# Optimization experiments

Hardware: AMD Instinct MI355X
Metric: run time of the kernel (lower is better)

The kernel has to match this reference:

```python
import jax, jax.numpy as jnp
import numpy as np

NUM_LAYER = 5
EMB = 256
N = 100000
E = 300000
SELF_LOOP_BOND = 4
BN_EPS = 1e-5


def setup_inputs() -> dict:
    key = jax.random.key(0)
    ks = jax.random.split(key, 16)
    f = lambda k, shape: jax.random.normal(k, shape, jnp.float32) * 0.02
    return {
        "x_atom": jax.random.randint(ks[0], (N,), 0, 120),
        "x_chir": jax.random.randint(ks[1], (N,), 0, 3),
        "edge_index": jax.random.randint(ks[2], (2, E), 0, N),
        "edge_bond": jax.random.randint(ks[3], (E,), 0, 4),
        "edge_dir": jax.random.randint(ks[4], (E,), 0, 3),
        "atom_emb": f(ks[5], (120, EMB)),
        "chir_emb": f(ks[6], (3, EMB)),
        "bond_embs": f(ks[7], (NUM_LAYER, 6, EMB)),
        "dir_embs": f(ks[8], (NUM_LAYER, 3, EMB)),
        "W1s": f(ks[9], (NUM_LAYER, 2 * EMB, EMB)),
        "b1s": f(ks[10], (NUM_LAYER, 2 * EMB)),
        "W2s": f(ks[11], (NUM_LAYER, EMB, 2 * EMB)),
        "b2s": f(ks[12], (NUM_LAYER, EMB)),
        "bn_w": jnp.ones((NUM_LAYER, EMB), jnp.float32),
        "bn_b": jnp.zeros((NUM_LAYER, EMB), jnp.float32),
    }


def reference(x_atom, x_chir, edge_index, edge_bond, edge_dir,
              atom_emb, chir_emb, bond_embs, dir_embs,
              W1s, b1s, W2s, b2s, bn_w, bn_b):
    n = x_atom.shape[0]
    src, dst = edge_index[0], edge_index[1]
    # add self loops (edge_attr = [4, 0] for each node)
    loop = jnp.arange(n)
    src_full = jnp.concatenate([src, loop])          # [E+N]
    dst_full = jnp.concatenate([dst, loop])          # [E+N]
    bond_full = jnp.concatenate([edge_bond, jnp.full((n,), SELF_LOOP_BOND, edge_bond.dtype)])
    dir_full = jnp.concatenate([edge_dir, jnp.zeros((n,), edge_dir.dtype)])

    # initial node features: atom + chirality embeddings
    h = atom_emb[x_atom] + chir_emb[x_chir]          # [N, EMB]

    for l in range(NUM_LAYER):
        # per-layer edge embeddings (bond type + bond direction)
        e_emb = bond_embs[l][bond_full] + dir_embs[l][dir_full]   # [E+N, EMB]
        # message = x_j + edge_attr; aggregate = scatter-add to dst
        msg = h[src_full] + e_emb                                  # gather
        agg = jax.ops.segment_sum(msg, dst_full, num_segments=n)  # scatter-add
        # update MLP: Linear(EMB->2EMB) -> ReLU -> Linear(2EMB->EMB)
        hmid = jax.nn.relu(agg @ W1s[l].T + b1s[l])                # [N, 2EMB]
        h2 = hmid @ W2s[l].T + b2s[l]                              # [N, EMB]
        # batch norm (training mode: batch statistics, biased variance)
        mean = h2.mean(axis=0)
        var = h2.var(axis=0)
        h2 = (h2 - mean) * jax.lax.rsqrt(var + BN_EPS) * bn_w[l] + bn_b[l]
        # relu on all but last layer; dropout with p=0 is identity
        if l < NUM_LAYER - 1:
            h2 = jax.nn.relu(h2)
        h = h2
    # JK == 'last'
    return h
```

## Files before the change

kernel.cpp:

```cpp
#include <hip/hip_runtime.h>

#define EMB 256
#define NLAYER 5
#define CHUNK 1024

typedef unsigned int u32;
typedef unsigned short u16;

typedef __bf16 bf16x8 __attribute__((ext_vector_type(8)));
typedef float f32x4 __attribute__((ext_vector_type(4)));

__device__ __forceinline__ float bf2f(u16 u) {
    union { u32 i; float f; } x; x.i = ((u32)u) << 16; return x.f;
}
__device__ __forceinline__ u16 f2bf(float f) {
    union { float f; u32 i; } x; x.f = f;
    u32 r = x.i + 0x7FFFu + ((x.i >> 16) & 1u);
    return (u16)(r >> 16);
}
__device__ __forceinline__ void unpack4(uint2 p, float* o) {
    union { u32 i; float f; } a, b, c, d;
    a.i = p.x << 16; b.i = p.x & 0xFFFF0000u;
    c.i = p.y << 16; d.i = p.y & 0xFFFF0000u;
    o[0] = a.f; o[1] = b.f; o[2] = c.f; o[3] = d.f;
}

__global__ void k_detect(const u32* __restrict__ bnw_raw, int* __restrict__ flag) {
    if (threadIdx.x == 0 && blockIdx.x == 0)
        *flag = (bnw_raw[0] == 0x3F803F80u) ? 1 : 0;
}

struct Cvt { const void* s; u16* d; int n; };
struct CvtTab { Cvt t[10]; };

__global__ void k_convert(CvtTab tab, const int* __restrict__ flag, int maxn) {
    int f = *flag;
    int stride = gridDim.x * blockDim.x;
    for (int i = blockIdx.x * blockDim.x + threadIdx.x; i < maxn; i += stride) {
        for (int j = 0; j < 10; j++) {
            if (i < tab.t[j].n) {
                u16 v;
                if (f) v = ((const u16*)tab.t[j].s)[i];
                else   v = f2bf(((const float*)tab.t[j].s)[i]);
                tab.t[j].d[i] = v;
            }
        }
    }
}

__global__ void k_zero(u32* p, int n) {
    int i = blockIdx.x * blockDim.x + threadIdx.x;
    if (i < n) p[i] = 0u;
}

__global__ void k_hist(const int* __restrict__ eidx, const int* __restrict__ ebond,
                       const int* __restrict__ edir,
                       u32* __restrict__ cnt, u32* __restrict__ cntb, u32* __restrict__ cntd, int E) {
    int e = blockIdx.x * blockDim.x + threadIdx.x;
    if (e >= E) return;
    int dst = eidx[E + e];
    atomicAdd(&cnt[dst], 1u);
    atomicAdd(&cntb[dst * 4 + ebond[e]], 1u);
    atomicAdd(&cntd[dst * 3 + edir[e]], 1u);
}

__global__ void k_chunksum(const u32* __restrict__ cnt, u32* __restrict__ partial, int N) {
    int b = blockIdx.x, t = threadIdx.x;
    int base = b * CHUNK + t * 4;
    u32 s = 0;
    for (int i = 0; i < 4; i++) { int idx = base + i; if (idx < N) s += cnt[idx]; }
    __shared__ u32 red[256];
    red[t] = s; __syncthreads();
    for (int o = 128; o > 0; o >>= 1) { if (t < o) red[t] += red[t + o]; __syncthreads(); }
    if (t == 0) partial[b] = red[0];
}

__global__ void k_scanpartial(u32* partial, u32* indptr, int nch, int N) {
    if (threadIdx.x == 0 && blockIdx.x == 0) {
        u32 run = 0;
        for (int i = 0; i < nch; i++) { u32 x = partial[i]; partial[i] = run; run += x; }
        indptr[N] = run;
    }
}

__global__ void k_chunkscan(const u32* __restrict__ cnt, const u32* __restrict__ partial,
                            u32* __restrict__ indptr, u32* __restrict__ fillp, int N) {
    int b = blockIdx.x, t = threadIdx.x;
    int base = b * CHUNK + t * 4;
    u32 c[4]; u32 tsum = 0;
    for (int i = 0; i < 4; i++) { int idx = base + i; c[i] = (idx < N) ? cnt[idx] : 0u; tsum += c[i]; }
    __shared__ u32 sc[256];
    sc[t] = tsum; __syncthreads();
    for (int o = 1; o < 256; o <<= 1) {
        u32 x = (t >= o) ? sc[t - o] : 0u;
        __syncthreads();
        sc[t] += x;
        __syncthreads();
    }
    u32 run = partial[b] + sc[t] - tsum;
    for (int i = 0; i < 4; i++) {
        int idx = base + i;
        if (idx < N) { indptr[idx] = run; fillp[idx] = run; }
        run += c[i];
    }
}

__global__ void k_fill(const int* __restrict__ eidx, u32* __restrict__ fillp,
                       u32* __restrict__ srcs, int E) {
    int e = blockIdx.x * blockDim.x + threadIdx.x;
    if (e >= E) return;
    int dst = eidx[E + e];
    u32 pos = atomicAdd(&fillp[dst], 1u);
    srcs[pos] = (u32)eidx[e];
}

__global__ void k_h0(const int* __restrict__ xa, const int* __restrict__ xc,
                     const u16* __restrict__ aemb, const u16* __restrict__ cemb,
                     u16* __restrict__ H, int N) {
    int wave = threadIdx.x >> 6, lane = threadIdx.x & 63;
    int v = blockIdx.x * 4 + wave;
    if (v >= N) return;
    int a = xa[v], c = xc[v];
    int c4 = lane * 4;
    uint2 pa = *(const uint2*)(aemb + (size_t)a * EMB + c4);
    uint2 pc = *(const uint2*)(cemb + (size_t)c * EMB + c4);
    float fa[4], fc[4];
    unpack4(pa, fa); unpack4(pc, fc);
    ushort4 ov;
    ov.x = f2bf(fa[0] + fc[0]); ov.y = f2bf(fa[1] + fc[1]);
    ov.z = f2bf(fa[2] + fc[2]); ov.w = f2bf(fa[3] + fc[3]);
    *(ushort4*)(H + (size_t)v * EMB + c4) = ov;
}

__global__ void k_scatter(const u16* __restrict__ H, const u32* __restrict__ indptr,
                          const u32* __restrict__ srcs,
                          const u32* __restrict__ cntb, const u32* __restrict__ cntd,
                          const u16* __restrict__ bemb, const u16* __restrict__ demb,
                          const float* __restrict__ scsh, int relu,
                          u16* __restrict__ AGG, int N) {
    int wave = threadIdx.x >> 6, lane = threadIdx.x & 63;
    int v = blockIdx.x * 4 + wave;
    if (v >= N) return;
    int c4 = lane * 4;
    float sc[4] = {1.f, 1.f, 1.f, 1.f}, sh[4] = {0.f, 0.f, 0.f, 0.f};
    if (scsh) {
        float4 s0 = *(const float4*)(scsh + c4);
        float4 s1 = *(const float4*)(scsh + 256 + c4);
        sc[0] = s0.x; sc[1] = s0.y; sc[2] = s0.z; sc[3] = s0.w;
        sh[0] = s1.x; sh[1] = s1.y; sh[2] = s1.z; sh[3] = s1.w;
    }
    float acc[4] = {0.f, 0.f, 0.f, 0.f};
    u32 beg = indptr[v], end = indptr[v + 1];
    for (u32 e = beg; e < end; e++) {
        u32 s = srcs[e];
        uint2 p = *(const uint2*)(H + (size_t)s * EMB + c4);
        float f[4]; unpack4(p, f);
        for (int i = 0; i < 4; i++) {
            float y = f[i] * sc[i] + sh[i];
            if (relu) y = fmaxf(y, 0.f);
            acc[i] += y;
        }
    }
    {
        uint2 p = *(const uint2*)(H + (size_t)v * EMB + c4);
        float f[4]; unpack4(p, f);
        for (int i = 0; i < 4; i++) {
            float y = f[i] * sc[i] + sh[i];
            if (relu) y = fmaxf(y, 0.f);
            acc[i] += y;
        }
    }
    float cb[5];
    cb[0] = (float)cntb[v * 4 + 0]; cb[1] = (float)cntb[v * 4 + 1];
    cb[2] = (float)cntb[v * 4 + 2]; cb[3] = (float)cntb[v * 4 + 3]; cb[4] = 1.f;
    float cd[3];
    cd[0] = (float)cntd[v * 3 + 0] + 1.f; cd[1] = (float)cntd[v * 3 + 1]; cd[2] = (float)cntd[v * 3 + 2];
    for (int b = 0; b < 5; b++) {
        uint2 p = *(const uint2*)(bemb + b * EMB + c4);
        float f[4]; unpack4(p, f);
        for (int i = 0; i < 4; i++) acc[i] += cb[b] * f[i];
    }
    for (int d = 0; d < 3; d++) {
        uint2 p = *(const uint2*)(demb + d * EMB + c4);
        float f[4]; unpack4(p, f);
        for (int i = 0; i < 4; i++) acc[i] += cd[d] * f[i];
    }
    ushort4 ov;
    ov.x = f2bf(acc[0]); ov.y = f2bf(acc[1]); ov.z = f2bf(acc[2]); ov.w = f2bf(acc[3]);
    *(ushort4*)(AGG + (size_t)v * EMB + c4) = ov;
}

#define KP1 264
#define KB1 40

__global__ __launch_bounds__(256) void k_gemm1(
    const u16* __restrict__ A, const u16* __restrict__ W1, const u16* __restrict__ bias,
    u16* __restrict__ HM, int M) {
    __shared__ __align__(16) u16 As[128 * KP1];
    __shared__ __align__(16) u16 Bs[128 * KB1];
    int m0 = blockIdx.x * 128;
    int t = threadIdx.x;
    int wave = t >> 6, lane = t & 63;
    int wm = (wave >> 1) * 64, wn = (wave & 1) * 64;
    int lr = lane & 15, quad = lane >> 4;

    for (int it = 0; it < 16; it++) {
        int ci = t + it * 256;
        int r = ci >> 5, kc = (ci & 31) * 8;
        int gr = m0 + r; if (gr > M - 1) gr = M - 1;
        *(uint4*)(As + r * KP1 + kc) = *(const uint4*)(A + (size_t)gr * 256 + kc);
    }
    __syncthreads();

    for (int nc = 0; nc < 4; nc++) {
        int n0 = nc * 128;
        f32x4 acc[4][4];
        for (int i = 0; i < 4; i++)
            for (int j = 0; j < 4; j++)
                acc[i][j] = (f32x4){0.f, 0.f, 0.f, 0.f};
        for (int ks = 0; ks < 256; ks += 32) {
            __syncthreads();
            for (int it = 0; it < 2; it++) {
                int ci = t + it * 256;
                int r = ci >> 2, kc = (ci & 3) * 8;
                *(uint4*)(Bs + r * KB1 + kc) = *(const uint4*)(W1 + (size_t)(n0 + r) * 256 + ks + kc);
            }
            __syncthreads();
            bf16x8 af[4], bfr[4];
            for (int i = 0; i < 4; i++)
                af[i] = *(const bf16x8*)(As + (wm + i * 16 + lr) * KP1 + ks + quad * 8);
            for (int j = 0; j < 4; j++)
                bfr[j] = *(const bf16x8*)(Bs + (wn + j * 16 + lr) * KB1 + quad * 8);
            for (int i = 0; i < 4; i++)
                for (int j = 0; j < 4; j++)
                    acc[i][j] = __builtin_amdgcn_mfma_f32_16x16x32_bf16(af[i], bfr[j], acc[i][j], 0, 0, 0);
        }
        for (int j = 0; j < 4; j++) {
            int gn = n0 + wn + j * 16 + lr;
            float bv = bf2f(bias[gn]);
            for (int i = 0; i < 4; i++) {
                int mbase = m0 + wm + i * 16 + quad * 4;
                for (int r = 0; r < 4; r++) {
                    int gm = mbase + r;
                    if (gm < M) {
                        float v = fmaxf(acc[i][j][r] + bv, 0.f);
                        HM[(size_t)gm * 512 + gn] = f2bf(v);
                    }
                }
            }
        }
    }
}

#define LSTR 80

__global__ __launch_bounds__(256) void k_gemm2(
    const u16* __restrict__ A, const u16* __restrict__ B, const u16* __restrict__ bias,
    u16* __restrict__ C, float* __restrict__ S, int M) {
    __shared__ __align__(16) u16 As[128 * LSTR];
    __shared__ __align__(16) u16 Bs[128 * LSTR];
    int n0 = blockIdx.x * 128;
    int m0 = blockIdx.y * 128;
    int t = threadIdx.x;
    int wave = t >> 6, lane = t & 63;
    int wm = (wave >> 1) * 64, wn = (wave & 1) * 64;
    int lr = lane & 15, quad = lane >> 4;

    f32x4 acc[4][4];
    for (int i = 0; i < 4; i++)
        for (int j = 0; j < 4; j++)
            acc[i][j] = (f32x4){0.f, 0.f, 0.f, 0.f};

    for (int k0 = 0; k0 < 512; k0 += 64) {
        for (int it = 0; it < 4; it++) {
            int ci = t + it * 256;
            int r = ci >> 3, kc = (ci & 7) * 8;
            int gr = m0 + r; if (gr > M - 1) gr = M - 1;
            *(uint4*)(As + r * LSTR + kc) = *(const uint4*)(A + (size_t)gr * 512 + k0 + kc);
            *(uint4*)(Bs + r * LSTR + kc) = *(const uint4*)(B + (size_t)(n0 + r) * 512 + k0 + kc);
        }
        __syncthreads();
        for (int ks = 0; ks < 64; ks += 32) {
            bf16x8 af[4], bfr[4];
            for (int i = 0; i < 4; i++)
                af[i] = *(const bf16x8*)(As + (wm + i * 16 + lr) * LSTR + ks + quad * 8);
            for (int j = 0; j < 4; j++)
                bfr[j] = *(const bf16x8*)(Bs + (wn + j * 16 + lr) * LSTR + ks + quad * 8);
            for (int i = 0; i < 4; i++)
                for (int j = 0; j < 4; j++)
                    acc[i][j] = __builtin_amdgcn_mfma_f32_16x16x32_bf16(af[i], bfr[j], acc[i][j], 0, 0, 0);
        }
        __syncthreads();
    }
    for (int j = 0; j < 4; j++) {
        int gn = n0 + wn + j * 16 + lr;
        float bv = bf2f(bias[gn]);
        float s = 0.f, q = 0.f;
        for (int i = 0; i < 4; i++) {
            int mbase = m0 + wm + i * 16 + quad * 4;
            for (int r = 0; r < 4; r++) {
                int gm = mbase + r;
                if (gm < M) {
                    float v = acc[i][j][r] + bv;
                    C[(size_t)gm * 256 + gn] = f2bf(v);
                    s += v; q += v * v;
                }
            }
        }
        s += __shfl_xor(s, 16, 64); s += __shfl_xor(s, 32, 64);
        q += __shfl_xor(q, 16, 64); q += __shfl_xor(q, 32, 64);
        if (quad == 0) {
            atomicAdd(&S[gn], s);
            atomicAdd(&S[256 + gn], q);
        }
    }
}

__global__ void k_finalize(const float* __restrict__ S, const u16* __restrict__ bnw,
                           const u16* __restrict__ bnb, float* __restrict__ scsh, float invN) {
    int c = threadIdx.x;
    float mean = S[c] * invN;
    float var = S[256 + c] * invN - mean * mean;
    var = fmaxf(var, 0.f);
    float inv = rsqrtf(var + 1e-5f);
    float sc = bf2f(bnw[c]) * inv;
    scsh[c] = sc;
    scsh[256 + c] = bf2f(bnb[c]) - mean * sc;
}

__global__ void k_out(const u16* __restrict__ H2, const float* __restrict__ scsh,
                      void* __restrict__ out, const int* __restrict__ flag, int N) {
    int wave = threadIdx.x >> 6, lane = threadIdx.x & 63;
    int v = blockIdx.x * 4 + wave;
    if (v >= N) return;
    int c4 = lane * 4;
    float4 s0 = *(const float4*)(scsh + c4);
    float4 s1 = *(const float4*)(scsh + 256 + c4);
    uint2 p = *(const uint2*)(H2 + (size_t)v * EMB + c4);
    float f[4]; unpack4(p, f);
    float o0 = f[0] * s0.x + s1.x;
    float o1 = f[1] * s0.y + s1.y;
    float o2 = f[2] * s0.z + s1.z;
    float o3 = f[3] * s0.w + s1.w;
    if (*flag) {
        ushort4 ov;
        ov.x = f2bf(o0); ov.y = f2bf(o1); ov.z = f2bf(o2); ov.w = f2bf(o3);
        *(ushort4*)((u16*)out + (size_t)v * EMB + c4) = ov;
    } else {
        float4 ov = make_float4(o0, o1, o2, o3);
        *(float4*)((float*)out + (size_t)v * EMB + c4) = ov;
    }
}

extern "C" void kernel_launch(void* const* d_in, const int* in_sizes, int n_in,
                              void* d_out, int out_size, void* d_ws, size_t ws_size,
                              hipStream_t stream) {
    const int* x_atom = (const int*)d_in[0];
    const int* x_chir = (const int*)d_in[1];
    const int* eidx   = (const int*)d_in[2];
    const int* ebond  = (const int*)d_in[3];
    const int* edir   = (const int*)d_in[4];

    const int N = in_sizes[0];
    const int E = in_sizes[3];

    char* p = (char*)d_ws;
    size_t off = 0;
    auto alloc = [&](size_t bytes) -> void* {
        void* r = p + off;
        off += bytes;
        off = (off + 255) & ~(size_t)255;
        return r;
    };
    u16* X   = (u16*)alloc((size_t)N * EMB * 2);
    u16* Y   = (u16*)alloc((size_t)N * EMB * 2);
    u16* HM  = (u16*)alloc((size_t)N * 512 * 2);
    u32* cz  = (u32*)alloc(((size_t)8 * N + NLAYER * 512) * 4);
    u32* cnt  = cz;
    u32* cntb = cz + N;
    u32* cntd = cz + 5 * (size_t)N;
    float* stats5 = (float*)(cz + 8 * (size_t)N);
    u32* indptr = (u32*)alloc((size_t)(N + 1) * 4);
    u32* fillp  = (u32*)alloc((size_t)N * 4);
    u32* srcs   = (u32*)alloc((size_t)E * 4);
    u32* partial = (u32*)alloc(256 * 4);
    float* scsh  = (float*)alloc(512 * 4);
    int* flag    = (int*)alloc(256);

    int csz[10] = {120 * EMB, 3 * EMB, NLAYER * 6 * EMB, NLAYER * 3 * EMB,
                   NLAYER * 512 * EMB, NLAYER * 512, NLAYER * EMB * 512, NLAYER * EMB,
                   NLAYER * EMB, NLAYER * EMB};
    u16* cbuf[10];
    for (int j = 0; j < 10; j++) cbuf[j] = (u16*)alloc((size_t)csz[j] * 2);
    u16* atom_emb  = cbuf[0];
    u16* chir_emb  = cbuf[1];
    u16* bond_embs = cbuf[2];
    u16* dir_embs  = cbuf[3];
    u16* W1s = cbuf[4];
    u16* b1s = cbuf[5];
    u16* W2s = cbuf[6];
    u16* b2s = cbuf[7];
    u16* bnw = cbuf[8];
    u16* bnb = cbuf[9];

    const int nodeBlocks = (N + 3) / 4;
    const int nch = (N + CHUNK - 1) / CHUNK;

    k_detect<<<1, 64, 0, stream>>>((const u32*)d_in[13], flag);
    {
        CvtTab tab;
        int maxn = 0;
        for (int j = 0; j < 10; j++) {
            tab.t[j].s = d_in[5 + j];
            tab.t[j].d = cbuf[j];
            tab.t[j].n = csz[j];
            if (csz[j] > maxn) maxn = csz[j];
        }
        k_convert<<<(maxn + 255) / 256, 256, 0, stream>>>(tab, flag, maxn);
    }

    {
        int z = 8 * N + NLAYER * 512;
        k_zero<<<(z + 255) / 256, 256, 0, stream>>>(cz, z);
    }
    k_hist<<<(E + 255) / 256, 256, 0, stream>>>(eidx, ebond, edir, cnt, cntb, cntd, E);
    k_chunksum<<<nch, 256, 0, stream>>>(cnt, partial, N);
    k_scanpartial<<<1, 64, 0, stream>>>(partial, indptr, nch, N);
    k_chunkscan<<<nch, 256, 0, stream>>>(cnt, partial, indptr, fillp, N);
    k_fill<<<(E + 255) / 256, 256, 0, stream>>>(eidx, fillp, srcs, E);

    k_h0<<<nodeBlocks, 256, 0, stream>>>(x_atom, x_chir, atom_emb, chir_emb, X, N);

    u16* H = X;
    u16* A = Y;
    const int mTiles = (N + 127) / 128;
    for (int l = 0; l < NLAYER; l++) {
        const u16* bemb = bond_embs + (size_t)l * 6 * EMB;
        const u16* demb = dir_embs + (size_t)l * 3 * EMB;
        const u16* W1 = W1s + (size_t)l * 512 * EMB;
        const u16* B1 = b1s + (size_t)l * 512;
        const u16* W2 = W2s + (size_t)l * EMB * 512;
        const u16* B2 = b2s + (size_t)l * EMB;
        float* stats = stats5 + (size_t)l * 512;

        k_scatter<<<nodeBlocks, 256, 0, stream>>>(H, indptr, srcs, cntb, cntd, bemb, demb,
                                                  (l == 0) ? nullptr : scsh, (l == 0) ? 0 : 1,
                                                  A, N);
        k_gemm1<<<mTiles, 256, 0, stream>>>(A, W1, B1, HM, N);
        {
            dim3 g(2, mTiles);
            k_gemm2<<<g, 256, 0, stream>>>(HM, W2, B2, A, stats, N);
        }
        k_finalize<<<1, 256, 0, stream>>>(stats, bnw + (size_t)l * EMB, bnb + (size_t)l * EMB,
                                          scsh, 1.0f / (float)N);
        u16* tmp = H; H = A; A = tmp;
    }

    k_out<<<nodeBlocks, 256, 0, stream>>>(H, scsh, d_out, flag, N);
}
```

Baseline: 1.284 ms.

## Restructure GEMM tiling to 64-row blocks with direct global B loads and slotted BN stats

```diff
diff --git a/kernel.cpp b/kernel.cpp
--- a/kernel.cpp
+++ b/kernel.cpp
@@ -3,6 +3,7 @@
 #define EMB 256
 #define NLAYER 5
 #define CHUNK 1024
+#define NSLOT 64
 
 typedef unsigned int u32;
 typedef unsigned short u16;
@@ -191,20 +192,17 @@
 }
 
 #define KP1 264
-#define KB1 40
-
-__global__ __launch_bounds__(256) void k_gemm1(
+
+__global__ __launch_bounds__(256, 2) void k_gemm1(
     const u16* __restrict__ A, const u16* __restrict__ W1, const u16* __restrict__ bias,
     u16* __restrict__ HM, int M) {
-    __shared__ __align__(16) u16 As[128 * KP1];
-    __shared__ __align__(16) u16 Bs[128 * KB1];
-    int m0 = blockIdx.x * 128;
+    __shared__ __align__(16) u16 As[64 * KP1];
+    int m0 = blockIdx.x * 64;
     int t = threadIdx.x;
     int wave = t >> 6, lane = t & 63;
-    int wm = (wave >> 1) * 64, wn = (wave & 1) * 64;
     int lr = lane & 15, quad = lane >> 4;
 
-    for (int it = 0; it < 16; it++) {
+    for (int it = 0; it < 8; it++) {
         int ci = t + it * 256;
         int r = ci >> 5, kc = (ci & 31) * 8;
         int gr = m0 + r; if (gr > M - 1) gr = M - 1;
@@ -212,92 +210,78 @@
     }
     __syncthreads();
 
-    for (int nc = 0; nc < 4; nc++) {
-        int n0 = nc * 128;
-        f32x4 acc[4][4];
+    int nbase = wave * 128;
+    f32x4 acc[4][8];
+    for (int i = 0; i < 4; i++)
+        for (int j = 0; j < 8; j++)
+            acc[i][j] = (f32x4){0.f, 0.f, 0.f, 0.f};
+
+    for (int ks = 0; ks < 256; ks += 32) {
+        bf16x8 af[4], bfr[8];
         for (int i = 0; i < 4; i++)
-            for (int j = 0; j < 4; j++)
-                acc[i][j] = (f32x4){0.f, 0.f, 0.f, 0.f};
-        for (int ks = 0; ks < 256; ks += 32) {
-            __syncthreads();
-            for (int it = 0; it < 2; it++) {
-                int ci = t + it * 256;
-                int r = ci >> 2, kc = (ci & 3) * 8;
-                *(uint4*)(Bs + r * KB1 + kc) = *(const uint4*)(W1 + (size_t)(n0 + r) * 256 + ks + kc);
+            af[i] = *(const bf16x8*)(As + (i * 16 + lr) * KP1 + ks + quad * 8);
+        for (int j = 0; j < 8; j++)
+            bfr[j] = *(const bf16x8*)(W1 + (size_t)(nbase + j * 16 + lr) * 256 + ks + quad * 8);
+        for (int i = 0; i < 4; i++)
+            for (int j = 0; j < 8; j++)
+                acc[i][j] = __builtin_amdgcn_mfma_f32_16x16x32_bf16(af[i], bfr[j], acc[i][j], 0, 0, 0);
+    }
+    for (int j = 0; j < 8; j++) {
+        int gn = nbase + j * 16 + lr;
+        float bv = bf2f(bias[gn]);
+        for (int i = 0; i < 4; i++) {
+            int mbase = m0 + i * 16 + quad * 4;
+            for (int r = 0; r < 4; r++) {
+                int gm = mbase + r;
+                if (gm < M)
+                    HM[(size_t)gm * 512 + gn] = f2bf(fmaxf(acc[i][j][r] + bv, 0.f));
             }
-            __syncthreads();
-            bf16x8 af[4], bfr[4];
-            for (int i = 0; i < 4; i++)
-                af[i] = *(const bf16x8*)(As + (wm + i * 16 + lr) * KP1 + ks + quad * 8);
-            for (int j = 0; j < 4; j++)
-                bfr[j] = *(const bf16x8*)(Bs + (wn + j * 16 + lr) * KB1 + quad * 8);
-            for (int i = 0; i < 4; i++)
-                for (int j = 0; j < 4; j++)
-                    acc[i][j] = __builtin_amdgcn_mfma_f32_16x16x32_bf16(af[i], bfr[j], acc[i][j], 0, 0, 0);
-        }
-        for (int j = 0; j < 4; j++) {
-            int gn = n0 + wn + j * 16 + lr;
-            float bv = bf2f(bias[gn]);
-            for (int i = 0; i < 4; i++) {
-                int mbase = m0 + wm + i * 16 + quad * 4;
-                for (int r = 0; r < 4; r++) {
-                    int gm = mbase + r;
-                    if (gm < M) {
-                        float v = fmaxf(acc[i][j][r] + bv, 0.f);
-                        HM[(size_t)gm * 512 + gn] = f2bf(v);
-                    }
-                }
-            }
-        }
-    }
-}
-
-#define LSTR 80
-
-__global__ __launch_bounds__(256) void k_gemm2(
-    const u16* __restrict__ A, const u16* __restrict__ B, const u16* __restrict__ bias,
+        }
+    }
+}
+
+#define KP2 520
+
+__global__ __launch_bounds__(256, 2) void k_gemm2(
+    const u16* __restrict__ A, const u16* __restrict__ W2, const u16* __restrict__ bias,
     u16* __restrict__ C, float* __restrict__ S, int M) {
-    __shared__ __align__(16) u16 As[128 * LSTR];
-    __shared__ __align__(16) u16 Bs[128 * LSTR];
-    int n0 = blockIdx.x * 128;
-    int m0 = blockIdx.y * 128;
+    __shared__ __align__(16) u16 As[64 * KP2];
+    int m0 = blockIdx.x * 64;
     int t = threadIdx.x;
     int wave = t >> 6, lane = t & 63;
-    int wm = (wave >> 1) * 64, wn = (wave & 1) * 64;
     int lr = lane & 15, quad = lane >> 4;
 
+    for (int it = 0; it < 16; it++) {
+        int ci = t + it * 256;
+        int r = ci >> 6, kc = (ci & 63) * 8;
+        int gr = m0 + r; if (gr > M - 1) gr = M - 1;
+        *(uint4*)(As + r * KP2 + kc) = *(const uint4*)(A + (size_t)gr * 512 + kc);
+    }
+    __syncthreads();
+
+    int nbase = wave * 64;
     f32x4 acc[4][4];
     for (int i = 0; i < 4; i++)
         for (int j = 0; j < 4; j++)
             acc[i][j] = (f32x4){0.f, 0.f, 0.f, 0.f};
 
-    for (int k0 = 0; k0 < 512; k0 += 64) {
-        for (int it = 0; it < 4; it++) {
-            int ci = t + it * 256;
-            int r = ci >> 3, kc = (ci & 7) * 8;
-            int gr = m0 + r; if (gr > M - 1) gr = M - 1;
-            *(uint4*)(As + r * LSTR + kc) = *(const uint4*)(A + (size_t)gr * 512 + k0 + kc);
-            *(uint4*)(Bs + r * LSTR + kc) = *(const uint4*)(B + (size_t)(n0 + r) * 512 + k0 + kc);
-        }
-        __syncthreads();
-        for (int ks = 0; ks < 64; ks += 32) {
-            bf16x8 af[4], bfr[4];
-            for (int i = 0; i < 4; i++)
-                af[i] = *(const bf16x8*)(As + (wm + i * 16 + lr) * LSTR + ks + quad * 8);
+    for (int ks = 0; ks < 512; ks += 32) {
+        bf16x8 af[4], bfr[4];
+        for (int i = 0; i < 4; i++)
+            af[i] = *(const bf16x8*)(As + (i * 16 + lr) * KP2 + ks + quad * 8);
+        for (int j = 0; j < 4; j++)
+            bfr[j] = *(const bf16x8*)(W2 + (size_t)(nbase + j * 16 + lr) * 512 + ks + quad * 8);
+        for (int i = 0; i < 4; i++)
             for (int j = 0; j < 4; j++)
-                bfr[j] = *(const bf16x8*)(Bs + (wn + j * 16 + lr) * LSTR + ks + quad * 8);
-            for (int i = 0; i < 4; i++)
-                for (int j = 0; j < 4; j++)
-                    acc[i][j] = __builtin_amdgcn_mfma_f32_16x16x32_bf16(af[i], bfr[j], acc[i][j], 0, 0, 0);
-        }
-        __syncthreads();
-    }
+                acc[i][j] = __builtin_amdgcn_mfma_f32_16x16x32_bf16(af[i], bfr[j], acc[i][j], 0, 0, 0);
+    }
+    float* Sslot = S + (size_t)(blockIdx.x & (NSLOT - 1)) * 512;
     for (int j = 0; j < 4; j++) {
-        int gn = n0 + wn + j * 16 + lr;
+        int gn = nbase + j * 16 + lr;
         float bv = bf2f(bias[gn]);
         float s = 0.f, q = 0.f;
         for (int i = 0; i < 4; i++) {
-            int mbase = m0 + wm + i * 16 + quad * 4;
+            int mbase = m0 + i * 16 + quad * 4;
             for (int r = 0; r < 4; r++) {
                 int gm = mbase + r;
                 if (gm < M) {
@@ -310,8 +294,8 @@
         s += __shfl_xor(s, 16, 64); s += __shfl_xor(s, 32, 64);
         q += __shfl_xor(q, 16, 64); q += __shfl_xor(q, 32, 64);
         if (quad == 0) {
-            atomicAdd(&S[gn], s);
-            atomicAdd(&S[256 + gn], q);
+            atomicAdd(&Sslot[gn], s);
+            atomicAdd(&Sslot[256 + gn], q);
         }
     }
 }
@@ -319,8 +303,13 @@
 __global__ void k_finalize(const float* __restrict__ S, const u16* __restrict__ bnw,
                            const u16* __restrict__ bnb, float* __restrict__ scsh, float invN) {
     int c = threadIdx.x;
-    float mean = S[c] * invN;
-    float var = S[256 + c] * invN - mean * mean;
+    float sum = 0.f, sq = 0.f;
+    for (int i = 0; i < NSLOT; i++) {
+        sum += S[(size_t)i * 512 + c];
+        sq  += S[(size_t)i * 512 + 256 + c];
+    }
+    float mean = sum * invN;
+    float var = sq * invN - mean * mean;
     var = fmaxf(var, 0.f);
     float inv = rsqrtf(var + 1e-5f);
     float sc = bf2f(bnw[c]) * inv;
@@ -375,7 +364,8 @@
     u16* X   = (u16*)alloc((size_t)N * EMB * 2);
     u16* Y   = (u16*)alloc((size_t)N * EMB * 2);
     u16* HM  = (u16*)alloc((size_t)N * 512 * 2);
-    u32* cz  = (u32*)alloc(((size_t)8 * N + NLAYER * 512) * 4);
+    const size_t statsWords = (size_t)NLAYER * NSLOT * 512;
+    u32* cz  = (u32*)alloc(((size_t)8 * N + statsWords) * 4);
     u32* cnt  = cz;
     u32* cntb = cz + N;
     u32* cntd = cz + 5 * (size_t)N;
@@ -420,8 +410,8 @@
     }
 
     {
-        int z = 8 * N + NLAYER * 512;
-        k_zero<<<(z + 255) / 256, 256, 0, stream>>>(cz, z);
+        size_t z = 8 * (size_t)N + statsWords;
+        k_zero<<<(int)((z + 255) / 256), 256, 0, stream>>>(cz, (int)z);
     }
     k_hist<<<(E + 255) / 256, 256, 0, stream>>>(eidx, ebond, edir, cnt, cntb, cntd, E);
     k_chunksum<<<nch, 256, 0, stream>>>(cnt, partial, N);
@@ -433,7 +423,7 @@
 
     u16* H = X;
     u16* A = Y;
-    const int mTiles = (N + 127) / 128;
+    const int mTiles64 = (N + 63) / 64;
     for (int l = 0; l < NLAYER; l++) {
         const u16* bemb = bond_embs + (size_t)l * 6 * EMB;
         const u16* demb = dir_embs + (size_t)l * 3 * EMB;
@@ -441,16 +431,13 @@
         const u16* B1 = b1s + (size_t)l * 512;
         const u16* W2 = W2s + (size_t)l * EMB * 512;
         const u16* B2 = b2s + (size_t)l * EMB;
-        float* stats = stats5 + (size_t)l * 512;
+        float* stats = stats5 + (size_t)l * NSLOT * 512;
 
         k_scatter<<<nodeBlocks, 256, 0, stream>>>(H, indptr, srcs, cntb, cntd, bemb, demb,
                                                   (l == 0) ? nullptr : scsh, (l == 0) ? 0 : 1,
                                                   A, N);
-        k_gemm1<<<mTiles, 256, 0, stream>>>(A, W1, B1, HM, N);
-        {
-            dim3 g(2, mTiles);
-            k_gemm2<<<g, 256, 0, stream>>>(HM, W2, B2, A, stats, N);
-        }
+        k_gemm1<<<mTiles64, 256, 0, stream>>>(A, W1, B1, HM, N);
+        k_gemm2<<<mTiles64, 256, 0, stream>>>(HM, W2, B2, A, stats, N);
         k_finalize<<<1, 256, 0, stream>>>(stats, bnw + (size_t)l * EMB, bnb + (size_t)l * EMB,
                                           scsh, 1.0f / (float)N);
         u16* tmp = H; H = A; A = tmp;
```

After: 1.473 ms. +14.8%, slower.
